# Kernel optimization log

Hardware: AMD Instinct MI355X
Metric: run time of the kernel (lower is better)

The kernel has to match this reference:

```python
import jax, jax.numpy as jnp
import numpy as np

N = 100000
E = 1600000
IN_DIM = 20
HID = 32
HEADS = 4
OUT = 64
NEG_SLOPE = 0.2


def _p(key, shape, scale=0.1):
    return jax.random.normal(key, shape, dtype=jnp.float32) * scale


def setup_inputs() -> dict:
    key = jax.random.key(0)
    ks = jax.random.split(key, 20)
    x = jax.random.normal(ks[0], (N, IN_DIM), dtype=jnp.float32)
    edge_index = jax.random.randint(ks[1], (2, E), 0, N, dtype=jnp.int32)
    edge_attr = jax.random.uniform(ks[2], (E, 1), dtype=jnp.float32)
    HC1 = HEADS * HID
    return {
        "x": x,
        "edge_index": edge_index,
        "edge_attr": edge_attr,
        "Wl1": _p(ks[3], (HC1, IN_DIM)), "bl1": jnp.zeros((HC1,), jnp.float32),
        "Wr1": _p(ks[4], (HC1, IN_DIM)), "br1": jnp.zeros((HC1,), jnp.float32),
        "We1": _p(ks[5], (HC1, 1)),
        "att1": _p(ks[6], (HEADS, HID)),
        "b1": jnp.zeros((HC1,), jnp.float32),
        "Wl2": _p(ks[7], (OUT, HC1)), "bl2": jnp.zeros((OUT,), jnp.float32),
        "Wr2": _p(ks[8], (OUT, HC1)), "br2": jnp.zeros((OUT,), jnp.float32),
        "We2": _p(ks[9], (OUT, 1)),
        "att2": _p(ks[10], (1, OUT)),
        "b2": jnp.zeros((OUT,), jnp.float32),
    }


def gatv2_conv(x, src, dst, edge_attr, Wl, bl, Wr, br, We, att, bias, heads, ch, concat):
    n = x.shape[0]
    # add self loops; edge_attr fill_value = mean (PyG default)
    loop = jnp.arange(n, dtype=src.dtype)
    src = jnp.concatenate([src, loop])
    dst = jnp.concatenate([dst, loop])
    ea_fill = jnp.broadcast_to(edge_attr.mean(axis=0, keepdims=True), (n, edge_attr.shape[1]))
    edge_attr = jnp.concatenate([edge_attr, ea_fill], axis=0)

    xl = (x @ Wl.T + bl).reshape(n, heads, ch)   # source transform [N,H,C]
    xr = (x @ Wr.T + br).reshape(n, heads, ch)   # target transform [N,H,C]
    ee = (edge_attr @ We.T).reshape(-1, heads, ch)  # edge embed [E',H,C]

    e = xl[src] + xr[dst] + ee                    # [E',H,C]
    e = jax.nn.leaky_relu(e, NEG_SLOPE)
    logits = jnp.einsum('ehc,hc->eh', e, att)     # [E',H]

    # segment softmax over destination nodes (every node has a self loop)
    mx = jax.ops.segment_max(logits, dst, num_segments=n)
    ex = jnp.exp(logits - mx[dst])
    denom = jax.ops.segment_sum(ex, dst, num_segments=n)
    alpha = ex / denom[dst]                       # [E',H]

    msg = xl[src] * alpha[:, :, None]             # [E',H,C]
    out = jax.ops.segment_sum(msg, dst, num_segments=n)  # [N,H,C]
    out = out.reshape(n, heads * ch) if concat else out.mean(axis=1)
    return out + bias


def reference(x, edge_index, edge_attr, Wl1, bl1, Wr1, br1, We1, att1, b1,
              Wl2, bl2, Wr2, br2, We2, att2, b2):
    src, dst = edge_index[0], edge_index[1]
    h = gatv2_conv(x, src, dst, edge_attr, Wl1, bl1, Wr1, br1, We1, att1, b1,
                   HEADS, HID, concat=True)
    h = jax.nn.elu(h)  # dropout is identity in eval mode
    out = gatv2_conv(h, src, dst, edge_attr, Wl2, bl2, Wr2, br2, We2, att2, b2,
                     1, OUT, concat=False)
    return out
```

## Files before the change

### kernel.cpp

```cpp
#include <hip/hip_runtime.h>
#include <cstdint>
#include <cstddef>

#define NNODES 100000
#define NEDGES 1600000
#define IN_DIM 20
#define HID    32
#define HEADS  4
#define HC1    128
#define OUTC   64
#define NEG    0.2f
#define LOG2E  1.4426950408889634f
#define NCHUNK ((NNODES + 255) / 256)
#define NBLK   ((NNODES + 63) / 64)

typedef _Float16 h2 __attribute__((ext_vector_type(2)));
typedef __fp16   hh2 __attribute__((ext_vector_type(2)));
union U4H { uint4 u; h2 h[4]; };
union U2H { uint2 u; h2 h[2]; };

#if __has_builtin(__builtin_amdgcn_fdot2)
#define FDOT2(a, b, c) __builtin_amdgcn_fdot2(__builtin_bit_cast(hh2, (a)), __builtin_bit_cast(hh2, (b)), (c), false)
#else
#define FDOT2(a, b, c) ((c) + (float)(a).x * (float)(b).x + (float)(a).y * (float)(b).y)
#endif

__global__ void k_sum(const float* __restrict__ ea, int n, float* __restrict__ out) {
    float s = 0.0f;
    for (int i = blockIdx.x * blockDim.x + threadIdx.x; i < n; i += gridDim.x * blockDim.x)
        s += ea[i];
    #pragma unroll
    for (int off = 32; off > 0; off >>= 1) s += __shfl_down(s, off, 64);
    __shared__ float ls[4];
    int lane = threadIdx.x & 63, wid = threadIdx.x >> 6;
    if (lane == 0) ls[wid] = s;
    __syncthreads();
    if (threadIdx.x == 0) {
        float t = ls[0] + ls[1] + ls[2] + ls[3];
        atomicAdd(out, t);
    }
}

__global__ void k_hist(const int* __restrict__ ei, int* __restrict__ cnt,
                       int* __restrict__ erank) {
    int e = blockIdx.x * blockDim.x + threadIdx.x;
    if (e < NEDGES) erank[e] = atomicAdd(&cnt[ei[NEDGES + e]], 1);
}

__global__ void k_scan_chunk(const int* __restrict__ cnt, int* __restrict__ rowptr,
                             int* __restrict__ csums) {
    __shared__ int s[256];
    int i = blockIdx.x * 256 + threadIdx.x;
    int v = (i < NNODES) ? cnt[i] : 0;
    s[threadIdx.x] = v;
    __syncthreads();
    for (int off = 1; off < 256; off <<= 1) {
        int t = (threadIdx.x >= off) ? s[threadIdx.x - off] : 0;
        __syncthreads();
        s[threadIdx.x] += t;
        __syncthreads();
    }
    if (i < NNODES) rowptr[i] = s[threadIdx.x] - v;
    if (threadIdx.x == 255) csums[blockIdx.x] = s[255];
}

__global__ void k_scan_tops(int* __restrict__ csums) {
    __shared__ int s[512];
    int v = (threadIdx.x < NCHUNK) ? csums[threadIdx.x] : 0;
    s[threadIdx.x] = v;
    __syncthreads();
    for (int off = 1; off < 512; off <<= 1) {
        int t = (threadIdx.x >= off) ? s[threadIdx.x - off] : 0;
        __syncthreads();
        s[threadIdx.x] += t;
        __syncthreads();
    }
    if (threadIdx.x < NCHUNK) csums[threadIdx.x] = s[threadIdx.x] - v;
}

__global__ void k_scan_add(int* __restrict__ rowptr, const int* __restrict__ csums) {
    int i = blockIdx.x * 256 + threadIdx.x;
    if (i < NNODES) rowptr[i] += csums[blockIdx.x];
    if (i == 0) rowptr[NNODES] = NEDGES;
}

__global__ void k_scatter(const int* __restrict__ ei, const float* __restrict__ ea,
                          const int* __restrict__ rowptr, const int* __restrict__ erank,
                          int2* __restrict__ cedge) {
    int e = blockIdx.x * blockDim.x + threadIdx.x;
    if (e >= NEDGES) return;
    int dst = ei[NEDGES + e];
    int pos = rowptr[dst] + erank[e];
    cedge[pos] = make_int2(ei[e], __float_as_int(ea[e]));
}

__global__ void k_dhist(const int* __restrict__ rowptr, int* __restrict__ bcnt,
                        int* __restrict__ nrank) {
    __shared__ int lcnt[64];
    __shared__ int lbase[64];
    int tid = threadIdx.x;
    if (tid < 64) lcnt[tid] = 0;
    __syncthreads();
    int n = blockIdx.x * 256 + tid;
    int d = 0, lr = 0;
    bool act = n < NNODES;
    if (act) {
        d = rowptr[n + 1] - rowptr[n];
        if (d > 63) d = 63;
        lr = atomicAdd(&lcnt[d], 1);
    }
    __syncthreads();
    if (tid < 64) lbase[tid] = lcnt[tid] ? atomicAdd(&bcnt[tid], lcnt[tid]) : 0;
    __syncthreads();
    if (act) nrank[n] = lbase[d] + lr;
}
__global__ void k_dscan(const int* __restrict__ bcnt, int* __restrict__ bbase) {
    int lane = threadIdx.x;
    int v = bcnt[lane];
    int sum = v;
    #pragma unroll
    for (int off = 1; off < 64; off <<= 1) {
        int t = __shfl_up(sum, off, 64);
        if (lane >= off) sum += t;
    }
    bbase[lane] = sum - v;
}
__global__ void k_place(const int* __restrict__ rowptr, const int* __restrict__ nrank,
                        const int* __restrict__ bbase, int* __restrict__ perm) {
    int n = blockIdx.x * 256 + threadIdx.x;
    if (n >= NNODES) return;
    int d = rowptr[n + 1] - rowptr[n];
    if (d > 63) d = 63;
    perm[bbase[d] + nrank[n]] = n;
}

__global__ void k_prep(const float* __restrict__ Wl1, const float* __restrict__ Wr1,
                       float* __restrict__ Bt1,
                       const float* __restrict__ Wl2, const float* __restrict__ Wr2,
                       float* __restrict__ Bt2,
                       const float* __restrict__ We1, const float* __restrict__ att1,
                       _Float16* __restrict__ Weh1, _Float16* __restrict__ Ath1,
                       const float* __restrict__ We2, const float* __restrict__ att2,
                       _Float16* __restrict__ Weh2, _Float16* __restrict__ Ath2) {
    int idx = blockIdx.x * 256 + threadIdx.x;
    if (idx < 16384) {
        int k = idx >> 7, c = idx & 127;
        Bt2[idx] = (c < 64) ? Wl2[c * HC1 + k] : Wr2[(c - 64) * HC1 + k];
    }
    int i1 = idx - 16384;
    if (i1 >= 0 && i1 < 5120) {
        int k = i1 >> 8, c = i1 & 255;
        Bt1[i1] = (c < 128) ? Wl1[c * IN_DIM + k] : Wr1[(c - 128) * IN_DIM + k];
    }
    int i2 = idx - (16384 + 5120);
    if (i2 >= 0 && i2 < 128) {
        Weh1[i2] = (_Float16)We1[i2];
        Ath1[i2] = (_Float16)(att1[i2] * LOG2E);
    }
    int i3 = idx - (16384 + 5120 + 128);
    if (i3 >= 0 && i3 < 64) {
        Weh2[i3] = (_Float16)We2[i3];
        Ath2[i3] = (_Float16)(att2[i3] * LOG2E);
    }
}

__global__ __launch_bounds__(256) void k_gemm1(
        const float* __restrict__ x, const float* __restrict__ Bt,
        const float* __restrict__ bl, const float* __restrict__ br,
        _Float16* __restrict__ xlh, _Float16* __restrict__ xrh) {
    __shared__ float sA[64 * IN_DIM];
    __shared__ float sB[IN_DIM * 256];
    int nb = blockIdx.x * 64;
    int tid = threadIdx.x;
    {
        size_t base = (size_t)nb * IN_DIM;
        size_t maxf = (size_t)NNODES * IN_DIM;
        for (int f = tid * 4; f < 64 * IN_DIM; f += 1024) {
            float4 v;
            if (base + f + 4 <= maxf) v = *(const float4*)(x + base + f);
            else                      v = *(const float4*)(x + maxf - 4);
            *(float4*)(sA + f) = v;
        }
    }
    for (int f = tid * 4; f < IN_DIM * 256; f += 1024)
        *(float4*)(sB + f) = *(const float4*)(Bt + f);
    __syncthreads();

    int tn = tid & 7, tc = tid >> 3;
    float acc[8][8];
    #pragma unroll
    for (int i = 0; i < 8; ++i)
        #pragma unroll
        for (int c = 0; c < 8; ++c) acc[i][c] = 0.0f;

    #pragma unroll
    for (int kt = 0; kt < 5; ++kt) {
        float4 a[8], b0[4], b1[4];
        #pragma unroll
        for (int i = 0; i < 8; ++i)
            a[i] = *(const float4*)(sA + (tn + 8 * i) * IN_DIM + kt * 4);
        #pragma unroll
        for (int j = 0; j < 4; ++j) {
            b0[j] = *(const float4*)(sB + (kt * 4 + j) * 256 + tc * 8);
            b1[j] = *(const float4*)(sB + (kt * 4 + j) * 256 + tc * 8 + 4);
        }
        #pragma unroll
        for (int i = 0; i < 8; ++i) {
            const float* ap = (const float*)&a[i];
            #pragma unroll
            for (int j = 0; j < 4; ++j) {
                float av = ap[j];
                const float* p0 = (const float*)&b0[j];
                const float* p1 = (const float*)&b1[j];
                #pragma unroll
                for (int c = 0; c < 4; ++c) {
                    acc[i][c]     += av * p0[c];
                    acc[i][c + 4] += av * p1[c];
                }
            }
        }
    }
    int c0 = tc * 8;
    float4 bias0, bias1;
    if (c0 < 128) {
        bias0 = *(const float4*)(bl + c0);
        bias1 = *(const float4*)(bl + c0 + 4);
    } else {
        bias0 = *(const float4*)(br + c0 - 128);
        bias1 = *(const float4*)(br + c0 - 124);
    }
    const float* q0 = (const float*)&bias0;
    const float* q1 = (const float*)&bias1;
    #pragma unroll
    for (int i = 0; i < 8; ++i) {
        int n = nb + tn + 8 * i;
        if (n >= NNODES) continue;
        float w[8];
        #pragma unroll
        for (int c = 0; c < 4; ++c) { w[c] = acc[i][c] + q0[c]; w[c + 4] = acc[i][c + 4] + q1[c]; }
        U4H ph;
        #pragma unroll
        for (int c = 0; c < 4; ++c) {
            h2 t; t.x = (_Float16)w[2 * c]; t.y = (_Float16)w[2 * c + 1];
            ph.h[c] = t;
        }
        if (c0 < 128) *(uint4*)(xlh + (size_t)n * HC1 + c0)       = ph.u;
        else          *(uint4*)(xrh + (size_t)n * HC1 + c0 - 128) = ph.u;
    }
}

__global__ __launch_bounds__(256) void k_gemm2(
        const _Float16* __restrict__ h1h, const float* __restrict__ Bt,
        const float* __restrict__ bl, const float* __restrict__ br,
        _Float16* __restrict__ xl2h, _Float16* __restrict__ xr2h) {
    __shared__ float sA[64 * 132];
    __shared__ float sB[32 * 128];
    int nb = blockIdx.x * 64;
    int tid = threadIdx.x;
    for (int idx = tid * 8; idx < 64 * HC1; idx += 2048) {
        int node = idx >> 7, k = idx & 127;
        int gn = nb + node; if (gn >= NNODES) gn = NNODES - 1;
        U4H v; v.u = *(const uint4*)(h1h + ((size_t)gn << 7) + k);
        float4 f0, f1;
        f0.x = (float)v.h[0].x; f0.y = (float)v.h[0].y;
        f0.z = (float)v.h[1].x; f0.w = (float)v.h[1].y;
        f1.x = (float)v.h[2].x; f1.y = (float)v.h[2].y;
        f1.z = (float)v.h[3].x; f1.w = (float)v.h[3].y;
        *(float4*)(sA + node * 132 + k)     = f0;
        *(float4*)(sA + node * 132 + k + 4) = f1;
    }
    int tn = tid & 7, tc = tid >> 3;
    float acc[8][4];
    #pragma unroll
    for (int i = 0; i < 8; ++i)
        #pragma unroll
        for (int c = 0; c < 4; ++c) acc[i][c] = 0.0f;

    for (int kc = 0; kc < 4; ++kc) {
        __syncthreads();
        for (int f = tid * 4; f < 32 * 128; f += 1024)
            *(float4*)(sB + f) = *(const float4*)(Bt + kc * 4096 + f);
        __syncthreads();
        #pragma unroll
        for (int ks = 0; ks < 8; ++ks) {
            int k0 = kc * 32 + ks * 4;
            float4 a[8], b[4];
            #pragma unroll
            for (int i = 0; i < 8; ++i)
                a[i] = *(const float4*)(sA + (tn + 8 * i) * 132 + k0);
            #pragma unroll
            for (int j = 0; j < 4; ++j)
                b[j] = *(const float4*)(sB + (ks * 4 + j) * 128 + tc * 4);
            #pragma unroll
            for (int i = 0; i < 8; ++i) {
                const float* ap = (const float*)&a[i];
                #pragma unroll
                for (int j = 0; j < 4; ++j) {
                    float av = ap[j];
                    const float* bp = (const float*)&b[j];
                    #pragma unroll
                    for (int c = 0; c < 4; ++c) acc[i][c] += av * bp[c];
                }
            }
        }
    }
    int c0 = tc * 4;
    float4 bias;
    if (c0 < 64) bias = *(const float4*)(bl + c0);
    else         bias = *(const float4*)(br + c0 - 64);
    const float* q = (const float*)&bias;
    #pragma unroll
    for (int i = 0; i < 8; ++i) {
        int n = nb + tn + 8 * i;
        if (n >= NNODES) continue;
        float w[4];
        #pragma unroll
        for (int c = 0; c < 4; ++c) w[c] = acc[i][c] + q[c];
        U2H ph;
        h2 t0; t0.x = (_Float16)w[0]; t0.y = (_Float16)w[1];
        h2 t1; t1.x = (_Float16)w[2]; t1.y = (_Float16)w[3];
        ph.h[0] = t0; ph.h[1] = t1;
        if (c0 < 64) *(uint2*)(xl2h + (size_t)n * OUTC + c0)      = ph.u;
        else         *(uint2*)(xr2h + (size_t)n * OUTC + c0 - 64) = ph.u;
    }
}

__global__ __launch_bounds__(256) void k_node1(
        const int* __restrict__ perm,
        const int* __restrict__ rowptr, const int2* __restrict__ cedge,
        const float* __restrict__ easum,
        const _Float16* __restrict__ xlh, const _Float16* __restrict__ xrh,
        const _Float16* __restrict__ Weh, const _Float16* __restrict__ Ath,
        const float* __restrict__ bias, _Float16* __restrict__ h1h) {
    int slot = blockIdx.x * 4 + (threadIdx.x >> 6);
    if (slot >= NNODES) return;
    int n = perm[slot];
    int lane = threadIdx.x & 63;
    int g = lane >> 4;
    int q = lane & 15;
    int c = q * 8;
    U4H xru; xru.u = *(const uint4*)(xrh + ((unsigned)n << 7) + c);
    U4H weu; weu.u = *(const uint4*)(Weh + c);
    U4H atu; atu.u = *(const uint4*)(Ath + c);
    h2 neg2; neg2.x = (_Float16)NEG; neg2.y = neg2.x;
    h2 zero; zero.x = (_Float16)0; zero.y = zero.x;
    h2 acc2[4] = { zero, zero, zero, zero };
    float s = 0.0f;
    int start = rowptr[n], deg = rowptr[n + 1] - start;

    {
        U4H xss; xss.u = *(const uint4*)(xlh + ((unsigned)n << 7) + c);
        float amean = easum[0] * (1.0f / (float)NEDGES);
        h2 a2; a2.x = (_Float16)amean; a2.y = a2.x;
        float p = 0.0f;
        #pragma unroll
        for (int j = 0; j < 4; ++j) {
            h2 e = xss.h[j] + (a2 * weu.h[j] + xru.h[j]);
            h2 l = __builtin_elementwise_max(e, neg2 * e);
            p = FDOT2(l, atu.h[j], p);
        }
        p += __shfl_xor(p, 1, 64);
        p += __shfl_xor(p, 2, 64);
        if (g == 0) {
            float pe = exp2f(p);
            s += pe;
            h2 pe2; pe2.x = (_Float16)pe; pe2.y = pe2.x;
            #pragma unroll
            for (int j = 0; j < 4; ++j) acc2[j] += pe2 * xss.h[j];
        }
    }

    if (deg > 0) {
        int dm1 = deg - 1;
        int2 epA = cedge[start + (g < dm1 ? g : dm1)];
        int2 epB = cedge[start + (4 + g < dm1 ? 4 + g : dm1)];
        for (int base = 0; base < deg; base += 8) {
            int2 cA = epA, cB = epB;
            int nxt = base + 8;
            if (nxt < deg) {
                int oA = nxt + g, oB = nxt + 4 + g;
                epA = cedge[start + (oA < dm1 ? oA : dm1)];
                epB = cedge[start + (oB < dm1 ? oB : dm1)];
            }
            U4H xA; xA.u = *(const uint4*)(xlh + ((unsigned)cA.x << 7) + c);
            U4H xB; xB.u = *(const uint4*)(xlh + ((unsigned)cB.x << 7) + c);
            {
                h2 a2; a2.x = (_Float16)__int_as_float(cA.y); a2.y = a2.x;
                float p = 0.0f;
                #pragma unroll
                for (int j = 0; j < 4; ++j) {
                    h2 e = xA.h[j] + (a2 * weu.h[j] + xru.h[j]);
                    h2 l = __builtin_elementwise_max(e, neg2 * e);
                    p = FDOT2(l, atu.h[j], p);
                }
                p += __shfl_xor(p, 1, 64);
                p += __shfl_xor(p, 2, 64);
                float pe = (base + g < deg) ? exp2f(p) : 0.0f;
                s += pe;
                h2 pe2; pe2.x = (_Float16)pe; pe2.y = pe2.x;
                #pragma unroll
                for (int j = 0; j < 4; ++j) acc2[j] += pe2 * xA.h[j];
            }
            {
                h2 a2; a2.x = (_Float16)__int_as_float(cB.y); a2.y = a2.x;
                float p = 0.0f;
                #pragma unroll
                for (int j = 0; j < 4; ++j) {
                    h2 e = xB.h[j] + (a2 * weu.h[j] + xru.h[j]);
                    h2 l = __builtin_elementwise_max(e, neg2 * e);
                    p = FDOT2(l, atu.h[j], p);
                }
                p += __shfl_xor(p, 1, 64);
                p += __shfl_xor(p, 2, 64);
                float pe = (base + 4 + g < deg) ? exp2f(p) : 0.0f;
                s += pe;
                h2 pe2; pe2.x = (_Float16)pe; pe2.y = pe2.x;
                #pragma unroll
                for (int j = 0; j < 4; ++j) acc2[j] += pe2 * xB.h[j];
            }
        }
    }
    #pragma unroll
    for (int off = 16; off <= 32; off <<= 1) {
        s += __shfl_xor(s, off, 64);
        #pragma unroll
        for (int j = 0; j < 4; ++j) {
            int lv = __builtin_bit_cast(int, acc2[j]);
            int t = __shfl_xor(lv, off, 64);
            acc2[j] += __builtin_bit_cast(h2, t);
        }
    }
    if (g == 0) {
        float inv = 1.0f / s;
        float4 bi0 = *(const float4*)(bias + c), bi1 = *(const float4*)(bias + c + 4);
        const float* bq = (const float*)&bi0;
        const float* br_ = (const float*)&bi1;
        float o[8];
        #pragma unroll
        for (int j = 0; j < 4; ++j) {
            o[2 * j]     = (float)acc2[j].x * inv + (j < 2 ? bq[2 * j]     : br_[2 * j - 4]);
            o[2 * j + 1] = (float)acc2[j].y * inv + (j < 2 ? bq[2 * j + 1] : br_[2 * j - 3]);
        }
        #pragma unroll
        for (int k = 0; k < 8; ++k) o[k] = o[k] > 0.0f ? o[k] : expm1f(o[k]);
        U4H ph;
        #pragma unroll
        for (int k = 0; k < 4; ++k) {
            h2 t; t.x = (_Float16)o[2 * k]; t.y = (_Float16)o[2 * k + 1];
            ph.h[k] = t;
        }
        *(uint4*)(h1h + ((unsigned)n << 7) + c) = ph.u;
    }
}

__global__ __launch_bounds__(256) void k_node2(
        const int* __restrict__ perm,
        const int* __restrict__ rowptr, const int2* __restrict__ cedge,
        const float* __restrict__ easum,
        const _Float16* __restrict__ xl2h, const _Float16* __restrict__ xr2h,
        const _Float16* __restrict__ Weh, const _Float16* __restrict__ Ath,
        const float* __restrict__ bias, float* __restrict__ out) {
    int slot = blockIdx.x * 4 + (threadIdx.x >> 6);
    if (slot >= NNODES) return;
    int n = perm[slot];
    int lane = threadIdx.x & 63;
    int g = lane >> 3;
    int q = lane & 7;
    int c = q * 8;
    U4H xru; xru.u = *(const uint4*)(xr2h + ((unsigned)n << 6) + c);
    U4H weu; weu.u = *(const uint4*)(Weh + c);
    U4H atu; atu.u = *(const uint4*)(Ath + c);
    h2 neg2; neg2.x = (_Float16)NEG; neg2.y = neg2.x;
    h2 zero; zero.x = (_Float16)0; zero.y = zero.x;
    h2 acc2[4] = { zero, zero, zero, zero };
    float s = 0.0f;
    int start = rowptr[n], deg = rowptr[n + 1] - start;

    {
        U4H xss; xss.u = *(const uint4*)(xl2h + ((unsigned)n << 6) + c);
        float amean = easum[0] * (1.0f / (float)NEDGES);
        h2 a2; a2.x = (_Float16)amean; a2.y = a2.x;
        float p = 0.0f;
        #pragma unroll
        for (int j = 0; j < 4; ++j) {
            h2 e = xss.h[j] + (a2 * weu.h[j] + xru.h[j]);
            h2 l = __builtin_elementwise_max(e, neg2 * e);
            p = FDOT2(l, atu.h[j], p);
        }
        p += __shfl_xor(p, 1, 64);
        p += __shfl_xor(p, 2, 64);
        p += __shfl_xor(p, 4, 64);
        if (g == 0) {
            float pe = exp2f(p);
            s += pe;
            h2 pe2; pe2.x = (_Float16)pe; pe2.y = pe2.x;
            #pragma unroll
            for (int j = 0; j < 4; ++j) acc2[j] += pe2 * xss.h[j];
        }
    }

    if (deg > 0) {
        int dm1 = deg - 1;
        int2 ep = cedge[start + (g < dm1 ? g : dm1)];
        for (int base = 0; base < deg; base += 8) {
            int2 cE = ep;
            int nxt = base + 8;
            if (nxt < deg) {
                int o = nxt + g;
                ep = cedge[start + (o < dm1 ? o : dm1)];
            }
            U4H xC; xC.u = *(const uint4*)(xl2h + ((unsigned)cE.x << 6) + c);
            h2 a2; a2.x = (_Float16)__int_as_float(cE.y); a2.y = a2.x;
            float p = 0.0f;
            #pragma unroll
            for (int j = 0; j < 4; ++j) {
                h2 e = xC.h[j] + (a2 * weu.h[j] + xru.h[j]);
                h2 l = __builtin_elementwise_max(e, neg2 * e);
                p = FDOT2(l, atu.h[j], p);
            }
            p += __shfl_xor(p, 1, 64);
            p += __shfl_xor(p, 2, 64);
            p += __shfl_xor(p, 4, 64);
            float pe = (base + g < deg) ? exp2f(p) : 0.0f;
            s += pe;
            h2 pe2; pe2.x = (_Float16)pe; pe2.y = pe2.x;
            #pragma unroll
            for (int j = 0; j < 4; ++j) acc2[j] += pe2 * xC.h[j];
        }
    }
    #pragma unroll
    for (int off = 8; off <= 32; off <<= 1) {
        s += __shfl_xor(s, off, 64);
        #pragma unroll
        for (int j = 0; j < 4; ++j) {
            int lv = __builtin_bit_cast(int, acc2[j]);
            int t = __shfl_xor(lv, off, 64);
            acc2[j] += __builtin_bit_cast(h2, t);
        }
    }
    if (g == 0) {
        float inv = 1.0f / s;
        float4 bi0 = *(const float4*)(bias + c), bi1 = *(const float4*)(bias + c + 4);
        const float* bq0 = (const float*)&bi0;
        const float* bq1 = (const float*)&bi1;
        float4 o0, o1;
        o0.x = (float)acc2[0].x * inv + bq0[0];  o0.y = (float)acc2[0].y * inv + bq0[1];
        o0.z = (float)acc2[1].x * inv + bq0[2];  o0.w = (float)acc2[1].y * inv + bq0[3];
        o1.x = (float)acc2[2].x * inv + bq1[0];  o1.y = (float)acc2[2].y * inv + bq1[1];
        o1.z = (float)acc2[3].x * inv + bq1[2];  o1.w = (float)acc2[3].y * inv + bq1[3];
        float4* op = (float4*)(out + (size_t)n * OUTC + c);
        op[0] = o0; op[1] = o1;
    }
}

extern "C" void kernel_launch(void* const* d_in, const int* in_sizes, int n_in,
                              void* d_out, int out_size, void* d_ws, size_t ws_size,
                              hipStream_t stream) {
    (void)in_sizes; (void)n_in; (void)out_size; (void)ws_size;
    const float* x    = (const float*)d_in[0];
    const int*   ei   = (const int*)d_in[1];
    const float* ea   = (const float*)d_in[2];
    const float* Wl1  = (const float*)d_in[3];
    const float* bl1  = (const float*)d_in[4];
    const float* Wr1  = (const float*)d_in[5];
    const float* br1  = (const float*)d_in[6];
    const float* We1  = (const float*)d_in[7];
    const float* att1 = (const float*)d_in[8];
    const float* b1   = (const float*)d_in[9];
    const float* Wl2  = (const float*)d_in[10];
    const float* bl2  = (const float*)d_in[11];
    const float* Wr2  = (const float*)d_in[12];
    const float* br2  = (const float*)d_in[13];
    const float* We2  = (const float*)d_in[14];
    const float* att2 = (const float*)d_in[15];
    const float* b2   = (const float*)d_in[16];
    float* out = (float*)d_out;

    char* wsb = (char*)d_ws;
    _Float16* xlh  = (_Float16*)wsb; wsb += (size_t)NNODES * HC1 * 2;
    _Float16* xrh  = (_Float16*)wsb; wsb += (size_t)NNODES * HC1 * 2;
    _Float16* h1h  = (_Float16*)wsb; wsb += (size_t)NNODES * HC1 * 2;
    int2*   cedge  = (int2*)wsb;     wsb += (size_t)NEDGES * 8;
    int*    erank  = (int*)wsb;      wsb += (size_t)NEDGES * 4;
    int*    cnt    = (int*)wsb;      wsb += (size_t)NNODES * 4;
    int*    rowptr = (int*)wsb;      wsb += ((size_t)(NNODES + 4) * 4);
    int*    perm   = (int*)wsb;      wsb += (size_t)NNODES * 4;
    int*    csums  = (int*)wsb;      wsb += 512 * 4;
    int*    bcnt   = (int*)wsb;      wsb += 64 * 4;
    int*    bbase  = (int*)wsb;      wsb += 64 * 4;
    float*  easum  = (float*)wsb;    wsb += 16;
    float*  Bt1    = (float*)wsb;    wsb += 20 * 256 * 4;
    float*  Bt2    = (float*)wsb;    wsb += 128 * 128 * 4;
    _Float16* Weh1 = (_Float16*)wsb; wsb += 128 * 2;
    _Float16* Ath1 = (_Float16*)wsb; wsb += 128 * 2;
    _Float16* Weh2 = (_Float16*)wsb; wsb += 64 * 2;
    _Float16* Ath2 = (_Float16*)wsb; wsb += 64 * 2;
    _Float16* xl2h = xlh;
    _Float16* xr2h = xrh;
    int* nrank = cnt;

    hipMemsetAsync(easum, 0, sizeof(float), stream);
    hipMemsetAsync(cnt, 0, (size_t)NNODES * 4, stream);
    hipMemsetAsync(bcnt, 0, 64 * 4, stream);

    k_sum<<<256, 256, 0, stream>>>(ea, NEDGES, easum);
    k_hist<<<(NEDGES + 255) / 256, 256, 0, stream>>>(ei, cnt, erank);
    k_prep<<<(16384 + 5120 + 128 + 64 + 255) / 256, 256, 0, stream>>>(
        Wl1, Wr1, Bt1, Wl2, Wr2, Bt2, We1, att1, Weh1, Ath1, We2, att2, Weh2, Ath2);
    k_scan_chunk<<<NCHUNK, 256, 0, stream>>>(cnt, rowptr, csums);
    k_scan_tops<<<1, 512, 0, stream>>>(csums);
    k_scan_add<<<NCHUNK, 256, 0, stream>>>(rowptr, csums);
    k_scatter<<<(NEDGES + 255) / 256, 256, 0, stream>>>(ei, ea, rowptr, erank, cedge);

    k_dhist<<<NCHUNK, 256, 0, stream>>>(rowptr, bcnt, nrank);
    k_dscan<<<1, 64, 0, stream>>>(bcnt, bbase);
    k_place<<<NCHUNK, 256, 0, stream>>>(rowptr, nrank, bbase, perm);

    k_gemm1<<<NBLK, 256, 0, stream>>>(x, Bt1, bl1, br1, xlh, xrh);
    k_node1<<<(NNODES + 3) / 4, 256, 0, stream>>>(perm, rowptr, cedge, easum,
                                                  xlh, xrh, Weh1, Ath1, b1, h1h);

    k_gemm2<<<NBLK, 256, 0, stream>>>(h1h, Bt2, bl2, br2, xl2h, xr2h);
    k_node2<<<(NNODES + 3) / 4, 256, 0, stream>>>(perm, rowptr, cedge, easum,
                                                  xl2h, xr2h, Weh2, Ath2, b2, out);
}
```

Baseline: 462.2 us.

## Fuse preprocessing kernels to cut launch count in CSR and degree-sort setup

Merges the edge-attribute sum, destination histogram and weight prep into one kernel, with per-block partial sums reduced later instead of a global atomic. Folds the degree bucketing into the chunk-scan kernel, since degree equals the count, and the bucket scan and permutation placement into the top-scan and scan-add kernels. Replaces three memsets with one contiguous memset. This removes roughly six kernel launches and several small passes over node arrays, at the cost of packing bucket and rank into one int (assumes rank < 2^20).

```diff
diff --git a/kernel.cpp b/kernel.cpp
--- a/kernel.cpp
+++ b/kernel.cpp
@@ -13,6 +13,9 @@
 #define LOG2E  1.4426950408889634f
 #define NCHUNK ((NNODES + 255) / 256)
 #define NBLK   ((NNODES + 63) / 64)
+#define EBLK   ((NEDGES + 255) / 256)
+#define PREPN  (16384 + 5120 + 128 + 64)
+#define PBLK   ((PREPN + 255) / 256)
 
 typedef _Float16 h2 __attribute__((ext_vector_type(2)));
 typedef __fp16   hh2 __attribute__((ext_vector_type(2)));
@@ -25,62 +28,133 @@
 #define FDOT2(a, b, c) ((c) + (float)(a).x * (float)(b).x + (float)(a).y * (float)(b).y)
 #endif
 
-__global__ void k_sum(const float* __restrict__ ea, int n, float* __restrict__ out) {
-    float s = 0.0f;
-    for (int i = blockIdx.x * blockDim.x + threadIdx.x; i < n; i += gridDim.x * blockDim.x)
-        s += ea[i];
-    #pragma unroll
-    for (int off = 32; off > 0; off >>= 1) s += __shfl_down(s, off, 64);
-    __shared__ float ls[4];
-    int lane = threadIdx.x & 63, wid = threadIdx.x >> 6;
-    if (lane == 0) ls[wid] = s;
-    __syncthreads();
-    if (threadIdx.x == 0) {
-        float t = ls[0] + ls[1] + ls[2] + ls[3];
-        atomicAdd(out, t);
-    }
-}
-
-__global__ void k_hist(const int* __restrict__ ei, int* __restrict__ cnt,
-                       int* __restrict__ erank) {
-    int e = blockIdx.x * blockDim.x + threadIdx.x;
-    if (e < NEDGES) erank[e] = atomicAdd(&cnt[ei[NEDGES + e]], 1);
+__global__ void k_histsum(const int* __restrict__ ei, const float* __restrict__ ea,
+                          int* __restrict__ cnt, int* __restrict__ erank,
+                          float* __restrict__ easpart,
+                          const float* __restrict__ Wl1, const float* __restrict__ Wr1,
+                          float* __restrict__ Bt1,
+                          const float* __restrict__ Wl2, const float* __restrict__ Wr2,
+                          float* __restrict__ Bt2,
+                          const float* __restrict__ We1, const float* __restrict__ att1,
+                          _Float16* __restrict__ Weh1, _Float16* __restrict__ Ath1,
+                          const float* __restrict__ We2, const float* __restrict__ att2,
+                          _Float16* __restrict__ Weh2, _Float16* __restrict__ Ath2) {
+    int blk = blockIdx.x;
+    int tid = threadIdx.x;
+    if (blk < EBLK) {
+        int e = blk * 256 + tid;
+        float v = 0.0f;
+        if (e < NEDGES) {
+            erank[e] = atomicAdd(&cnt[ei[NEDGES + e]], 1);
+            v = ea[e];
+        }
+        #pragma unroll
+        for (int off = 32; off > 0; off >>= 1) v += __shfl_down(v, off, 64);
+        __shared__ float ws4[4];
+        int lane = tid & 63, wid = tid >> 6;
+        if (lane == 0) ws4[wid] = v;
+        __syncthreads();
+        if (tid == 0) easpart[blk] = ws4[0] + ws4[1] + ws4[2] + ws4[3];
+    } else {
+        int idx = (blk - EBLK) * 256 + tid;
+        if (idx < 16384) {
+            int k = idx >> 7, c = idx & 127;
+            Bt2[idx] = (c < 64) ? Wl2[c * HC1 + k] : Wr2[(c - 64) * HC1 + k];
+        }
+        int i1 = idx - 16384;
+        if (i1 >= 0 && i1 < 5120) {
+            int k = i1 >> 8, c = i1 & 255;
+            Bt1[i1] = (c < 128) ? Wl1[c * IN_DIM + k] : Wr1[(c - 128) * IN_DIM + k];
+        }
+        int i2 = idx - (16384 + 5120);
+        if (i2 >= 0 && i2 < 128) {
+            Weh1[i2] = (_Float16)We1[i2];
+            Ath1[i2] = (_Float16)(att1[i2] * LOG2E);
+        }
+        int i3 = idx - (16384 + 5120 + 128);
+        if (i3 >= 0 && i3 < 64) {
+            Weh2[i3] = (_Float16)We2[i3];
+            Ath2[i3] = (_Float16)(att2[i3] * LOG2E);
+        }
+    }
 }
 
 __global__ void k_scan_chunk(const int* __restrict__ cnt, int* __restrict__ rowptr,
-                             int* __restrict__ csums) {
+                             int* __restrict__ csums,
+                             int* __restrict__ bcnt, int* __restrict__ nrankp) {
     __shared__ int s[256];
-    int i = blockIdx.x * 256 + threadIdx.x;
+    __shared__ int lcnt[64];
+    __shared__ int lbase[64];
+    int tid = threadIdx.x;
+    if (tid < 64) lcnt[tid] = 0;
+    int i = blockIdx.x * 256 + tid;
     int v = (i < NNODES) ? cnt[i] : 0;
-    s[threadIdx.x] = v;
+    s[tid] = v;
     __syncthreads();
     for (int off = 1; off < 256; off <<= 1) {
-        int t = (threadIdx.x >= off) ? s[threadIdx.x - off] : 0;
-        __syncthreads();
-        s[threadIdx.x] += t;
-        __syncthreads();
-    }
-    if (i < NNODES) rowptr[i] = s[threadIdx.x] - v;
-    if (threadIdx.x == 255) csums[blockIdx.x] = s[255];
-}
-
-__global__ void k_scan_tops(int* __restrict__ csums) {
+        int t = (tid >= off) ? s[tid - off] : 0;
+        __syncthreads();
+        s[tid] += t;
+        __syncthreads();
+    }
+    if (i < NNODES) rowptr[i] = s[tid] - v;
+    if (tid == 255) csums[blockIdx.x] = s[255];
+    int d = v > 63 ? 63 : v;
+    int lr = 0;
+    if (i < NNODES) lr = atomicAdd(&lcnt[d], 1);
+    __syncthreads();
+    if (tid < 64) lbase[tid] = lcnt[tid] ? atomicAdd(&bcnt[tid], lcnt[tid]) : 0;
+    __syncthreads();
+    if (i < NNODES) nrankp[i] = (d << 20) | (lbase[d] + lr);
+}
+
+__global__ void k_scan_tops(int* __restrict__ csums,
+                            const int* __restrict__ bcnt, int* __restrict__ bbase,
+                            const float* __restrict__ easpart, float* __restrict__ easum) {
     __shared__ int s[512];
-    int v = (threadIdx.x < NCHUNK) ? csums[threadIdx.x] : 0;
-    s[threadIdx.x] = v;
+    __shared__ float fs[512];
+    int tid = threadIdx.x;
+    int v = (tid < NCHUNK) ? csums[tid] : 0;
+    s[tid] = v;
+    float sv = 0.0f;
+    for (int i = tid; i < EBLK; i += 512) sv += easpart[i];
+    fs[tid] = sv;
     __syncthreads();
     for (int off = 1; off < 512; off <<= 1) {
-        int t = (threadIdx.x >= off) ? s[threadIdx.x - off] : 0;
-        __syncthreads();
-        s[threadIdx.x] += t;
-        __syncthreads();
-    }
-    if (threadIdx.x < NCHUNK) csums[threadIdx.x] = s[threadIdx.x] - v;
-}
-
-__global__ void k_scan_add(int* __restrict__ rowptr, const int* __restrict__ csums) {
+        int t = (tid >= off) ? s[tid - off] : 0;
+        __syncthreads();
+        s[tid] += t;
+        __syncthreads();
+    }
+    if (tid < NCHUNK) csums[tid] = s[tid] - v;
+    if (tid < 64) {
+        int b = bcnt[tid];
+        int sum = b;
+        #pragma unroll
+        for (int off = 1; off < 64; off <<= 1) {
+            int t = __shfl_up(sum, off, 64);
+            if (tid >= off) sum += t;
+        }
+        bbase[tid] = sum - b;
+    }
+    __syncthreads();
+    for (int off = 256; off > 0; off >>= 1) {
+        if (tid < off) fs[tid] += fs[tid + off];
+        __syncthreads();
+    }
+    if (tid == 0) easum[0] = fs[0];
+}
+
+__global__ void k_scan_add(int* __restrict__ rowptr, const int* __restrict__ csums,
+                           const int* __restrict__ nrankp, const int* __restrict__ bbase,
+                           int* __restrict__ perm) {
     int i = blockIdx.x * 256 + threadIdx.x;
-    if (i < NNODES) rowptr[i] += csums[blockIdx.x];
+    if (i < NNODES) {
+        rowptr[i] += csums[blockIdx.x];
+        int np = nrankp[i];
+        int d = np >> 20, r = np & 0xFFFFF;
+        perm[bbase[d] + r] = i;
+    }
     if (i == 0) rowptr[NNODES] = NEDGES;
 }
 
@@ -92,76 +166,6 @@
     int dst = ei[NEDGES + e];
     int pos = rowptr[dst] + erank[e];
     cedge[pos] = make_int2(ei[e], __float_as_int(ea[e]));
-}
-
-__global__ void k_dhist(const int* __restrict__ rowptr, int* __restrict__ bcnt,
-                        int* __restrict__ nrank) {
-    __shared__ int lcnt[64];
-    __shared__ int lbase[64];
-    int tid = threadIdx.x;
-    if (tid < 64) lcnt[tid] = 0;
-    __syncthreads();
-    int n = blockIdx.x * 256 + tid;
-    int d = 0, lr = 0;
-    bool act = n < NNODES;
-    if (act) {
-        d = rowptr[n + 1] - rowptr[n];
-        if (d > 63) d = 63;
-        lr = atomicAdd(&lcnt[d], 1);
-    }
-    __syncthreads();
-    if (tid < 64) lbase[tid] = lcnt[tid] ? atomicAdd(&bcnt[tid], lcnt[tid]) : 0;
-    __syncthreads();
-    if (act) nrank[n] = lbase[d] + lr;
-}
-__global__ void k_dscan(const int* __restrict__ bcnt, int* __restrict__ bbase) {
-    int lane = threadIdx.x;
-    int v = bcnt[lane];
-    int sum = v;
-    #pragma unroll
-    for (int off = 1; off < 64; off <<= 1) {
-        int t = __shfl_up(sum, off, 64);
-        if (lane >= off) sum += t;
-    }
-    bbase[lane] = sum - v;
-}
-__global__ void k_place(const int* __restrict__ rowptr, const int* __restrict__ nrank,
-                        const int* __restrict__ bbase, int* __restrict__ perm) {
-    int n = blockIdx.x * 256 + threadIdx.x;
-    if (n >= NNODES) return;
-    int d = rowptr[n + 1] - rowptr[n];
-    if (d > 63) d = 63;
-    perm[bbase[d] + nrank[n]] = n;
-}
-
-__global__ void k_prep(const float* __restrict__ Wl1, const float* __restrict__ Wr1,
-                       float* __restrict__ Bt1,
-                       const float* __restrict__ Wl2, const float* __restrict__ Wr2,
-                       float* __restrict__ Bt2,
-                       const float* __restrict__ We1, const float* __restrict__ att1,
-                       _Float16* __restrict__ Weh1, _Float16* __restrict__ Ath1,
-                       const float* __restrict__ We2, const float* __restrict__ att2,
-                       _Float16* __restrict__ Weh2, _Float16* __restrict__ Ath2) {
-    int idx = blockIdx.x * 256 + threadIdx.x;
-    if (idx < 16384) {
-        int k = idx >> 7, c = idx & 127;
-        Bt2[idx] = (c < 64) ? Wl2[c * HC1 + k] : Wr2[(c - 64) * HC1 + k];
-    }
-    int i1 = idx - 16384;
-    if (i1 >= 0 && i1 < 5120) {
-        int k = i1 >> 8, c = i1 & 255;
-        Bt1[i1] = (c < 128) ? Wl1[c * IN_DIM + k] : Wr1[(c - 128) * IN_DIM + k];
-    }
-    int i2 = idx - (16384 + 5120);
-    if (i2 >= 0 && i2 < 128) {
-        Weh1[i2] = (_Float16)We1[i2];
-        Ath1[i2] = (_Float16)(att1[i2] * LOG2E);
-    }
-    int i3 = idx - (16384 + 5120 + 128);
-    if (i3 >= 0 && i3 < 64) {
-        Weh2[i3] = (_Float16)We2[i3];
-        Ath2[i3] = (_Float16)(att2[i3] * LOG2E);
-    }
 }
 
 __global__ __launch_bounds__(256) void k_gemm1(
@@ -582,11 +586,14 @@
     _Float16* h1h  = (_Float16*)wsb; wsb += (size_t)NNODES * HC1 * 2;
     int2*   cedge  = (int2*)wsb;     wsb += (size_t)NEDGES * 8;
     int*    erank  = (int*)wsb;      wsb += (size_t)NEDGES * 4;
-    int*    cnt    = (int*)wsb;      wsb += (size_t)NNODES * 4;
+    int*    nrankp = (int*)wsb;      wsb += (size_t)NNODES * 4;
     int*    rowptr = (int*)wsb;      wsb += ((size_t)(NNODES + 4) * 4);
     int*    perm   = (int*)wsb;      wsb += (size_t)NNODES * 4;
     int*    csums  = (int*)wsb;      wsb += 512 * 4;
+    float*  easpart= (float*)wsb;    wsb += (size_t)EBLK * 4;
+    int*    cnt    = (int*)wsb;      wsb += (size_t)NNODES * 4;
     int*    bcnt   = (int*)wsb;      wsb += 64 * 4;
+    size_t  zbytes = (size_t)NNODES * 4 + 64 * 4;
     int*    bbase  = (int*)wsb;      wsb += 64 * 4;
     float*  easum  = (float*)wsb;    wsb += 16;
     float*  Bt1    = (float*)wsb;    wsb += 20 * 256 * 4;
@@ -597,24 +604,15 @@
     _Float16* Ath2 = (_Float16*)wsb; wsb += 64 * 2;
     _Float16* xl2h = xlh;
     _Float16* xr2h = xrh;
-    int* nrank = cnt;
-
-    hipMemsetAsync(easum, 0, sizeof(float), stream);
-    hipMemsetAsync(cnt, 0, (size_t)NNODES * 4, stream);
-    hipMemsetAsync(bcnt, 0, 64 * 4, stream);
-
-    k_sum<<<256, 256, 0, stream>>>(ea, NEDGES, easum);
-    k_hist<<<(NEDGES + 255) / 256, 256, 0, stream>>>(ei, cnt, erank);
-    k_prep<<<(16384 + 5120 + 128 + 64 + 255) / 256, 256, 0, stream>>>(
+
+    hipMemsetAsync(cnt, 0, zbytes, stream);
+
+    k_histsum<<<EBLK + PBLK, 256, 0, stream>>>(ei, ea, cnt, erank, easpart,
         Wl1, Wr1, Bt1, Wl2, Wr2, Bt2, We1, att1, Weh1, Ath1, We2, att2, Weh2, Ath2);
-    k_scan_chunk<<<NCHUNK, 256, 0, stream>>>(cnt, rowptr, csums);
-    k_scan_tops<<<1, 512, 0, stream>>>(csums);
-    k_scan_add<<<NCHUNK, 256, 0, stream>>>(rowptr, csums);
+    k_scan_chunk<<<NCHUNK, 256, 0, stream>>>(cnt, rowptr, csums, bcnt, nrankp);
+    k_scan_tops<<<1, 512, 0, stream>>>(csums, bcnt, bbase, easpart, easum);
+    k_scan_add<<<NCHUNK, 256, 0, stream>>>(rowptr, csums, nrankp, bbase, perm);
     k_scatter<<<(NEDGES + 255) / 256, 256, 0, stream>>>(ei, ea, rowptr, erank, cedge);
-
-    k_dhist<<<NCHUNK, 256, 0, stream>>>(rowptr, bcnt, nrank);
-    k_dscan<<<1, 64, 0, stream>>>(bcnt, bbase);
-    k_place<<<NCHUNK, 256, 0, stream>>>(rowptr, nrank, bbase, perm);
 
     k_gemm1<<<NBLK, 256, 0, stream>>>(x, Bt1, bl1, br1, xlh, xrh);
     k_node1<<<(NNODES + 3) / 4, 256, 0, stream>>>(perm, rowptr, cedge, easum,
```

Result: faster. 443.0 us, median of 2 (-4.1%).
